# Kernel tuning notes

Hardware: AMD Instinct MI355X
Metric: run time of the kernel (lower is better)

## Reference

```python
import jax, jax.numpy as jnp
import numpy as np

B, S, E, H = 16, 1024, 320, 8
DH = E // H  # 40


def _lin(x, W, b):
    return x @ W.T + b


def setup_inputs() -> dict:
    key = jax.random.key(0)
    ks = jax.random.split(key, 16)

    def w(k, shape, fan_in):
        return jax.random.normal(k, shape, dtype=jnp.float32) / np.float32(np.sqrt(fan_in))

    z = lambda n: jnp.zeros((n,), jnp.float32)
    return {
        "sequence_features": jax.random.normal(ks[0], (B, S, E), dtype=jnp.float32),
        # feature_processor (shared, applied twice): Linear(320,320)+ReLU+Linear(320,320)
        "fpW1": w(ks[1], (E, E), E), "fpb1": z(E),
        "fpW2": w(ks[2], (E, E), E), "fpb2": z(E),
        # MultiheadAttention(320, 8) in/out projections
        "Wq": w(ks[3], (E, E), E), "bq": z(E),
        "Wk": w(ks[4], (E, E), E), "bk": z(E),
        "Wv": w(ks[5], (E, E), E), "bv": z(E),
        "Wo": w(ks[6], (E, E), E), "bo": z(E),
        # contact MLP: Linear(320,160)+ReLU+Linear(160,1)
        "mW1": w(ks[7], (160, E), E), "mb1": z(160),
        "mW2": w(ks[8], (1, 160), 160), "mb2": z(1),
        # position_predictor: Linear(640,320)+ReLU+Linear(320,160)+ReLU+Linear(160,3)
        "pW1": w(ks[9], (E, 2 * E), 2 * E), "pb1": z(E),
        "pW2": w(ks[10], (160, E), E), "pb2": z(160),
        "pW3": w(ks[11], (3, 160), 160), "pb3": z(3),
    }


def _forward(x, fpW1, fpb1, fpW2, fpb2, Wq, bq, Wk, bk, Wv, bv, Wo, bo,
             mW1, mb1, mW2, mb2, pW1, pb1, pW2, pb2, pW3, pb3):
    # feature_processor (dropout = identity in eval)
    backbone = _lin(jax.nn.relu(_lin(x, fpW1, fpb1)), fpW2, fpb2)        # [B,S,E]
    side = _lin(jax.nn.relu(_lin(backbone, fpW1, fpb1)), fpW2, fpb2)     # [B,S,E]

    # MultiheadAttention with batch_first=False semantics: input is treated as
    # [L=B, N=S, E], i.e. attention mixes over the batch axis (dim 0).
    q = _lin(x, Wq, bq).reshape(B, S, H, DH)
    k = _lin(x, Wk, bk).reshape(B, S, H, DH)
    v = _lin(x, Wv, bv).reshape(B, S, H, DH)
    scale = np.float32(1.0 / np.sqrt(DH))
    scores = jnp.einsum("lshd,mshd->shlm", q, k) * scale                 # [S,H,B,B]
    attn = jax.nn.softmax(scores, axis=-1)
    ctx = jnp.einsum("shlm,mshd->lshd", attn, v).reshape(B, S, E)
    attn_out = _lin(ctx, Wo, bo)                                         # [B,S,E]

    # per-position MLP -> scalar; torch broadcast-assigns it across the row
    prob = _lin(jax.nn.relu(_lin(attn_out, mW1, mb1)), mW2, mb2)         # [B,S,1]
    contact_map = jnp.broadcast_to(prob, (B, S, S))                      # [B,S,S]

    # refinement loop is a no-op: output == position_predictor(cat(bb, sc))
    comb = jnp.concatenate([backbone, side], axis=-1)                    # [B,S,640]
    h = jax.nn.relu(_lin(comb, pW1, pb1))
    h = jax.nn.relu(_lin(h, pW2, pb2))
    refined = _lin(h, pW3, pb3)                                          # [B,S,3]
    return backbone, side, contact_map, refined


def reference(sequence_features, fpW1, fpb1, fpW2, fpb2, Wq, bq, Wk, bk, Wv, bv,
              Wo, bo, mW1, mb1, mW2, mb2, pW1, pb1, pW2, pb2, pW3, pb3):
    return _forward(sequence_features, fpW1, fpb1, fpW2, fpb2, Wq, bq, Wk, bk,
                    Wv, bv, Wo, bo, mW1, mb1, mW2, mb2, pW1, pb1, pW2, pb2, pW3, pb3)
```

## Files before the change

### kernel.cpp

```cpp
#include <hip/hip_runtime.h>
#include <math.h>


#define M_ROWS 16384

typedef float f32x4 __attribute__((ext_vector_type(4)));
typedef __bf16 bf16x8 __attribute__((ext_vector_type(8)));
typedef unsigned short ushort_t;

typedef const __attribute__((address_space(1))) void* gas_ptr;
typedef __attribute__((address_space(3))) void* las_ptr;

__device__ __forceinline__ unsigned int f2bf(float f) {
    union { float f; unsigned int u; } v; v.f = f;
    unsigned int u = v.u + 0x7FFFu + ((v.u >> 16) & 1u);
    return u >> 16;
}
__device__ __forceinline__ float bf2f(ushort_t s) {
    union { unsigned int u; float f; } v; v.u = ((unsigned int)s) << 16;
    return v.f;
}

template<int BN>
__device__ __forceinline__ void gemm_core(
    int tx, int ty,
    const ushort_t* __restrict__ X1, const ushort_t* __restrict__ X2,
    int ksplit, int K, const ushort_t* __restrict__ W,
    char* smem, f32x4 (*acc)[2])
{
    constexpr int BM = 128, BK = 64;
    constexpr int WROWS = (BN == 64) ? 2 : 4;
    constexpr int WCOLS = 4 / WROWS;
    constexpr int WM = BM / WROWS;
    constexpr int WN = BN / WCOLS;
    constexpr int MF = WM / 16;
    constexpr int NF = WN / 16;

    ushort_t* As = (ushort_t*)smem;
    ushort_t* Bs = As + BM * BK;

    const int tid  = threadIdx.x;
    const int wave = tid >> 6;
    const int lane = tid & 63;
    const int m0 = ty * BM;
    const int n0 = tx * BN;
    const int wr = wave / WCOLS;
    const int wc = wave % WCOLS;
    const int sr = lane >> 3;
    const int su = lane & 7;

    for (int k0 = 0; k0 < K; k0 += BK) {
        #pragma unroll
        for (int i = 0; i < (BM * BK * 2) / 4096; ++i) {
            const int c = i * 4 + wave;
            const int r = c * 8 + sr;
            const int gk = k0 + (su ^ (r & 7)) * 8;
            const ushort_t* src;
            if (gk < ksplit) src = X1 + (size_t)(m0 + r) * ksplit + gk;
            else             src = X2 + (size_t)(m0 + r) * (K - ksplit) + (gk - ksplit);
            __builtin_amdgcn_global_load_lds((gas_ptr)src, (las_ptr)&As[c * 512], 16, 0, 0);
        }
        #pragma unroll
        for (int i = 0; i < (BN * BK * 2) / 4096; ++i) {
            const int c = i * 4 + wave;
            const int r = c * 8 + sr;
            const int gk = k0 + (su ^ (r & 7)) * 8;
            const ushort_t* src = W + (size_t)(n0 + r) * K + gk;
            __builtin_amdgcn_global_load_lds((gas_ptr)src, (las_ptr)&Bs[c * 512], 16, 0, 0);
        }
        __syncthreads();

        #pragma unroll
        for (int s = 0; s < 2; ++s) {
            bf16x8 a[MF], b[NF];
            #pragma unroll
            for (int mf = 0; mf < MF; ++mf) {
                const int r  = wr * WM + mf * 16 + (lane & 15);
                const int lu = (s * 4 + (lane >> 4)) ^ (r & 7);
                a[mf] = *reinterpret_cast<const bf16x8*>(&As[r * 64 + lu * 8]);
            }
            #pragma unroll
            for (int nf = 0; nf < NF; ++nf) {
                const int r  = wc * WN + nf * 16 + (lane & 15);
                const int lu = (s * 4 + (lane >> 4)) ^ (r & 7);
                b[nf] = *reinterpret_cast<const bf16x8*>(&Bs[r * 64 + lu * 8]);
            }
            #pragma unroll
            for (int mf = 0; mf < MF; ++mf)
                #pragma unroll
                for (int nf = 0; nf < NF; ++nf)
                    acc[mf][nf] = __builtin_amdgcn_mfma_f32_16x16x32_bf16(
                        a[mf], b[nf], acc[mf][nf], 0, 0, 0);
        }
        __syncthreads();
    }
}

template<int BN, bool RELU>
__device__ __forceinline__ void gemm_store(
    int tx, int ty, f32x4 (*acc)[2], const float* __restrict__ bias,
    float* __restrict__ outF, ushort_t* __restrict__ outB, int N)
{
    constexpr int WROWS = (BN == 64) ? 2 : 4;
    constexpr int WCOLS = 4 / WROWS;
    constexpr int WM = 128 / WROWS;
    constexpr int WN = BN / WCOLS;
    constexpr int MF = WM / 16;

    const int tid  = threadIdx.x;
    const int wave = tid >> 6;
    const int lane = tid & 63;
    const int wr = wave / WCOLS;
    const int wc = wave % WCOLS;

    #pragma unroll
    for (int nf = 0; nf < 2; ++nf) {
        const int gn = tx * BN + wc * WN + nf * 16 + (lane & 15);
        const float bv = bias[gn];
        #pragma unroll
        for (int mf = 0; mf < MF; ++mf) {
            #pragma unroll
            for (int i = 0; i < 4; ++i) {
                const int gm = ty * 128 + wr * WM + mf * 16 + (lane >> 4) * 4 + i;
                float v = acc[mf][nf][i] + bv;
                if (RELU) v = fmaxf(v, 0.f);
                if (outF) outF[(size_t)gm * N + gn] = v;
                if (outB) outB[(size_t)gm * N + gn] = (ushort_t)f2bf(v);
            }
        }
    }
}

template<int BN, bool RELU>
__device__ __forceinline__ void gemm_full(
    int bid, int ntx,
    const ushort_t* X1, const ushort_t* X2, int ksplit, int K,
    const ushort_t* W, const float* bias,
    float* outF, ushort_t* outB, int N, char* smem)
{
    const int tx = bid % ntx, ty = bid / ntx;
    constexpr int MF = (BN == 64) ? 4 : 2;
    f32x4 acc[MF][2];
    #pragma unroll
    for (int i = 0; i < MF; ++i) { acc[i][0] = (f32x4)0.f; acc[i][1] = (f32x4)0.f; }
    gemm_core<BN>(tx, ty, X1, X2, ksplit, K, W, smem, acc);
    gemm_store<BN, RELU>(tx, ty, acc, bias, outF, outB, N);
}

__device__ __forceinline__ void attn_dev(
    int ab, const ushort_t* __restrict__ qkv, ushort_t* __restrict__ ctx, char* smem)
{
    float* q_s = (float*)smem;
    float* k_s = q_s + 16 * 40;
    float* v_s = k_s + 16 * 40;
    float* p_s = v_s + 16 * 40;

    const int s   = ab >> 3;
    const int h   = ab & 7;
    const int tid = threadIdx.x;
    const int hb  = h * 40;

    for (int idx = tid; idx < 16 * 40; idx += 256) {
        int l = idx / 40, d = idx % 40;
        size_t row = (size_t)(l * 1024 + s) * 960;
        q_s[idx] = bf2f(qkv[row + hb + d]);
        k_s[idx] = bf2f(qkv[row + 320 + hb + d]);
        v_s[idx] = bf2f(qkv[row + 640 + hb + d]);
    }
    __syncthreads();

    {
        const int l = tid >> 4, m = tid & 15;
        float sc = 0.f;
        #pragma unroll
        for (int d = 0; d < 40; ++d) sc += q_s[l * 40 + d] * k_s[m * 40 + d];
        sc *= 0.15811388300841897f;
        float mx = sc;
        #pragma unroll
        for (int off = 1; off < 16; off <<= 1) mx = fmaxf(mx, __shfl_xor(mx, off, 16));
        float e = expf(sc - mx);
        float sum = e;
        #pragma unroll
        for (int off = 1; off < 16; off <<= 1) sum += __shfl_xor(sum, off, 16);
        p_s[l * 16 + m] = e / sum;
    }
    __syncthreads();

    for (int idx = tid; idx < 16 * 40; idx += 256) {
        int l = idx / 40, d = idx % 40;
        float acc = 0.f;
        #pragma unroll
        for (int m = 0; m < 16; ++m) acc += p_s[l * 16 + m] * v_s[m * 40 + d];
        ctx[(size_t)(l * 1024 + s) * 320 + hb + d] = (ushort_t)f2bf(acc);
    }
}


__device__ __forceinline__ void stage64(
    const ushort_t* __restrict__ src, int row0, int ldk, int k0,
    ushort_t* dst, int wave, int sr, int su)
{
    #pragma unroll
    for (int i = 0; i < 2; ++i) {
        const int c = i * 4 + wave;
        const int r = c * 8 + sr;
        const int gk = k0 + (su ^ (r & 7)) * 8;
        __builtin_amdgcn_global_load_lds(
            (gas_ptr)(src + (size_t)(row0 + r) * ldk + gk),
            (las_ptr)&dst[c * 512], 16, 0, 0);
    }
}
__device__ __forceinline__ void stage32(
    const ushort_t* __restrict__ src, int row0, int ldk, int k0,
    ushort_t* dst, int wave, int sr, int su)
{
    const int r = wave * 8 + sr;
    const int gk = k0 + (su ^ (r & 7)) * 8;
    __builtin_amdgcn_global_load_lds(
        (gas_ptr)(src + (size_t)(row0 + r) * ldk + gk),
        (las_ptr)&dst[wave * 512], 16, 0, 0);
}

__device__ void fusedB_dev(
    int panel, const ushort_t* __restrict__ bbB,
    const ushort_t* __restrict__ fpW1b, const float* __restrict__ fpb1,
    const ushort_t* __restrict__ fpW2b, const float* __restrict__ fpb2,
    float* __restrict__ out_side, ushort_t* __restrict__ sideB, char* smem)
{
    ushort_t* tpan = (ushort_t*)smem;
    ushort_t* As   = tpan + 5 * 4096;
    ushort_t* Bs   = As + 4096;

    const int tid = threadIdx.x, wave = tid >> 6, lane = tid & 63;
    const int row0 = panel * 64;
    const int wr = wave >> 1, wc = wave & 1;
    const int sr = lane >> 3, su = lane & 7;

    for (int nb = 0; nb < 5; ++nb) {
        f32x4 acc[2][2];
        acc[0][0] = acc[0][1] = acc[1][0] = acc[1][1] = (f32x4)0.f;
        for (int k0 = 0; k0 < 320; k0 += 64) {
            stage64(bbB,   row0,    320, k0, As, wave, sr, su);
            stage64(fpW1b, nb * 64, 320, k0, Bs, wave, sr, su);
            __syncthreads();
            #pragma unroll
            for (int s = 0; s < 2; ++s) {
                bf16x8 a[2], b[2];
                #pragma unroll
                for (int mf = 0; mf < 2; ++mf) {
                    const int r  = wr * 32 + mf * 16 + (lane & 15);
                    const int lu = (s * 4 + (lane >> 4)) ^ (r & 7);
                    a[mf] = *reinterpret_cast<const bf16x8*>(&As[r * 64 + lu * 8]);
                }
                #pragma unroll
                for (int nf = 0; nf < 2; ++nf) {
                    const int r  = wc * 32 + nf * 16 + (lane & 15);
                    const int lu = (s * 4 + (lane >> 4)) ^ (r & 7);
                    b[nf] = *reinterpret_cast<const bf16x8*>(&Bs[r * 64 + lu * 8]);
                }
                #pragma unroll
                for (int mf = 0; mf < 2; ++mf)
                    #pragma unroll
                    for (int nf = 0; nf < 2; ++nf)
                        acc[mf][nf] = __builtin_amdgcn_mfma_f32_16x16x32_bf16(
                            a[mf], b[nf], acc[mf][nf], 0, 0, 0);
            }
            __syncthreads();
        }
        #pragma unroll
        for (int nf = 0; nf < 2; ++nf) {
            const int col = wc * 32 + nf * 16 + (lane & 15);
            const float bv = fpb1[nb * 64 + col];
            #pragma unroll
            for (int mf = 0; mf < 2; ++mf) {
                #pragma unroll
                for (int i = 0; i < 4; ++i) {
                    const int row = wr * 32 + mf * 16 + (lane >> 4) * 4 + i;
                    float v = fmaxf(acc[mf][nf][i] + bv, 0.f);
                    const int u = col >> 3;
                    tpan[nb * 4096 + row * 64 + ((u ^ (row & 7)) * 8) + (col & 7)]
                        = (ushort_t)f2bf(v);
                }
            }
        }
        __syncthreads();
    }

    for (int nb = 0; nb < 5; ++nb) {
        f32x4 acc[2][2];
        acc[0][0] = acc[0][1] = acc[1][0] = acc[1][1] = (f32x4)0.f;
        for (int kt = 0; kt < 5; ++kt) {
            stage64(fpW2b, nb * 64, 320, kt * 64, Bs, wave, sr, su);
            __syncthreads();
            #pragma unroll
            for (int s = 0; s < 2; ++s) {
                bf16x8 a[2], b[2];
                #pragma unroll
                for (int mf = 0; mf < 2; ++mf) {
                    const int r  = wr * 32 + mf * 16 + (lane & 15);
                    const int lu = (s * 4 + (lane >> 4)) ^ (r & 7);
                    a[mf] = *reinterpret_cast<const bf16x8*>(&tpan[kt * 4096 + r * 64 + lu * 8]);
                }
                #pragma unroll
                for (int nf = 0; nf < 2; ++nf) {
                    const int r  = wc * 32 + nf * 16 + (lane & 15);
                    const int lu = (s * 4 + (lane >> 4)) ^ (r & 7);
                    b[nf] = *reinterpret_cast<const bf16x8*>(&Bs[r * 64 + lu * 8]);
                }
                #pragma unroll
                for (int mf = 0; mf < 2; ++mf)
                    #pragma unroll
                    for (int nf = 0; nf < 2; ++nf)
                        acc[mf][nf] = __builtin_amdgcn_mfma_f32_16x16x32_bf16(
                            a[mf], b[nf], acc[mf][nf], 0, 0, 0);
            }
            __syncthreads();
        }
        #pragma unroll
        for (int nf = 0; nf < 2; ++nf) {
            const int gn = nb * 64 + wc * 32 + nf * 16 + (lane & 15);
            const float bv = fpb2[gn];
            #pragma unroll
            for (int mf = 0; mf < 2; ++mf) {
                #pragma unroll
                for (int i = 0; i < 4; ++i) {
                    const int gm = row0 + wr * 32 + mf * 16 + (lane >> 4) * 4 + i;
                    float v = acc[mf][nf][i] + bv;
                    out_side[(size_t)gm * 320 + gn] = v;
                    sideB[(size_t)gm * 320 + gn] = (ushort_t)f2bf(v);
                }
            }
        }
    }
}

__device__ void fusedC_dev(
    int panel, const ushort_t* __restrict__ bbB, const ushort_t* __restrict__ sideB,
    const ushort_t* __restrict__ pW1b, const float* __restrict__ pb1,
    const ushort_t* __restrict__ pW2b, const float* __restrict__ pb2,
    const float* __restrict__ pW3, const float* __restrict__ pb3,
    float* __restrict__ out_ref, char* smem)
{
    ushort_t* tpan = (ushort_t*)smem;
    ushort_t* As   = tpan + 5 * 4096;
    ushort_t* Bs   = As + 4096;

    const int tid = threadIdx.x, wave = tid >> 6, lane = tid & 63;
    const int row0 = panel * 64;
    const int wr = wave >> 1, wc = wave & 1;
    const int sr = lane >> 3, su = lane & 7;

    for (int nb = 0; nb < 5; ++nb) {
        f32x4 acc[2][2];
        acc[0][0] = acc[0][1] = acc[1][0] = acc[1][1] = (f32x4)0.f;
        for (int k0 = 0; k0 < 640; k0 += 64) {
            #pragma unroll
            for (int i = 0; i < 2; ++i) {
                const int c = i * 4 + wave;
                const int r = c * 8 + sr;
                const int gk = k0 + (su ^ (r & 7)) * 8;
                const ushort_t* src = (gk < 320)
                    ? bbB   + (size_t)(row0 + r) * 320 + gk
                    : sideB + (size_t)(row0 + r) * 320 + (gk - 320);
                __builtin_amdgcn_global_load_lds((gas_ptr)src, (las_ptr)&As[c * 512], 16, 0, 0);
            }
            stage64(pW1b, nb * 64, 640, k0, Bs, wave, sr, su);
            __syncthreads();
            #pragma unroll
            for (int s = 0; s < 2; ++s) {
                bf16x8 a[2], b[2];
                #pragma unroll
                for (int mf = 0; mf < 2; ++mf) {
                    const int r  = wr * 32 + mf * 16 + (lane & 15);
                    const int lu = (s * 4 + (lane >> 4)) ^ (r & 7);
                    a[mf] = *reinterpret_cast<const bf16x8*>(&As[r * 64 + lu * 8]);
                }
                #pragma unroll
                for (int nf = 0; nf < 2; ++nf) {
                    const int r  = wc * 32 + nf * 16 + (lane & 15);
                    const int lu = (s * 4 + (lane >> 4)) ^ (r & 7);
                    b[nf] = *reinterpret_cast<const bf16x8*>(&Bs[r * 64 + lu * 8]);
                }
                #pragma unroll
                for (int mf = 0; mf < 2; ++mf)
                    #pragma unroll
                    for (int nf = 0; nf < 2; ++nf)
                        acc[mf][nf] = __builtin_amdgcn_mfma_f32_16x16x32_bf16(
                            a[mf], b[nf], acc[mf][nf], 0, 0, 0);
            }
            __syncthreads();
        }
        #pragma unroll
        for (int nf = 0; nf < 2; ++nf) {
            const int col = wc * 32 + nf * 16 + (lane & 15);
            const float bv = pb1[nb * 64 + col];
            #pragma unroll
            for (int mf = 0; mf < 2; ++mf) {
                #pragma unroll
                for (int i = 0; i < 4; ++i) {
                    const int row = wr * 32 + mf * 16 + (lane >> 4) * 4 + i;
                    float v = fmaxf(acc[mf][nf][i] + bv, 0.f);
                    const int u = col >> 3;
                    tpan[nb * 4096 + row * 64 + ((u ^ (row & 7)) * 8) + (col & 7)]
                        = (ushort_t)f2bf(v);
                }
            }
        }
        __syncthreads();
    }

    float part[4][3];
    #pragma unroll
    for (int i = 0; i < 4; ++i) { part[i][0] = part[i][1] = part[i][2] = 0.f; }

    for (int ct = 0; ct < 5; ++ct) {
        f32x4 acc[2];
        acc[0] = acc[1] = (f32x4)0.f;
        for (int kt = 0; kt < 5; ++kt) {
            stage32(pW2b, ct * 32, 320, kt * 64, Bs, wave, sr, su);
            __syncthreads();
            #pragma unroll
            for (int s = 0; s < 2; ++s) {
                bf16x8 a, b[2];
                {
                    const int r  = wave * 16 + (lane & 15);
                    const int lu = (s * 4 + (lane >> 4)) ^ (r & 7);
                    a = *reinterpret_cast<const bf16x8*>(&tpan[kt * 4096 + r * 64 + lu * 8]);
                }
                #pragma unroll
                for (int nf = 0; nf < 2; ++nf) {
                    const int r  = nf * 16 + (lane & 15);
                    const int lu = (s * 4 + (lane >> 4)) ^ (r & 7);
                    b[nf] = *reinterpret_cast<const bf16x8*>(&Bs[r * 64 + lu * 8]);
                }
                #pragma unroll
                for (int nf = 0; nf < 2; ++nf)
                    acc[nf] = __builtin_amdgcn_mfma_f32_16x16x32_bf16(a, b[nf], acc[nf], 0, 0, 0);
            }
            __syncthreads();
        }
        #pragma unroll
        for (int nf = 0; nf < 2; ++nf) {
            const int col = ct * 32 + nf * 16 + (lane & 15);
            const float bv = pb2[col];
            #pragma unroll
            for (int i = 0; i < 4; ++i) {
                float v = fmaxf(acc[nf][i] + bv, 0.f);
                #pragma unroll
                for (int n = 0; n < 3; ++n)
                    part[i][n] += v * pW3[n * 160 + col];
            }
        }
    }
    #pragma unroll
    for (int off = 8; off; off >>= 1)
        #pragma unroll
        for (int i = 0; i < 4; ++i)
            #pragma unroll
            for (int n = 0; n < 3; ++n)
                part[i][n] += __shfl_xor(part[i][n], off, 16);
    if ((lane & 15) == 0) {
        #pragma unroll
        for (int i = 0; i < 4; ++i) {
            const int row = row0 + wave * 16 + (lane >> 4) * 4 + i;
            #pragma unroll
            for (int n = 0; n < 3; ++n)
                out_ref[(size_t)row * 3 + n] = part[i][n] + pb3[n];
        }
    }
}

__device__ void fusedD_dev(
    int panel, const ushort_t* __restrict__ aoB,
    const ushort_t* __restrict__ mW1b, const float* __restrict__ mb1,
    const float* __restrict__ mW2, const float* __restrict__ mb2,
    float* __restrict__ out_cm, char* smem)
{
    ushort_t* As = (ushort_t*)smem;
    ushort_t* Bs = As + 4096;
    float* probs = (float*)(Bs + 2048);

    const int tid = threadIdx.x, wave = tid >> 6, lane = tid & 63;
    const int row0 = panel * 64;
    const int sr = lane >> 3, su = lane & 7;

    float part[4] = {0.f, 0.f, 0.f, 0.f};

    for (int ct = 0; ct < 5; ++ct) {
        f32x4 acc[2];
        acc[0] = acc[1] = (f32x4)0.f;
        for (int k0 = 0; k0 < 320; k0 += 64) {
            stage64(aoB,  row0,    320, k0, As, wave, sr, su);
            stage32(mW1b, ct * 32, 320, k0, Bs, wave, sr, su);
            __syncthreads();
            #pragma unroll
            for (int s = 0; s < 2; ++s) {
                bf16x8 a, b[2];
                {
                    const int r  = wave * 16 + (lane & 15);
                    const int lu = (s * 4 + (lane >> 4)) ^ (r & 7);
                    a = *reinterpret_cast<const bf16x8*>(&As[r * 64 + lu * 8]);
                }
                #pragma unroll
                for (int nf = 0; nf < 2; ++nf) {
                    const int r  = nf * 16 + (lane & 15);
                    const int lu = (s * 4 + (lane >> 4)) ^ (r & 7);
                    b[nf] = *reinterpret_cast<const bf16x8*>(&Bs[r * 64 + lu * 8]);
                }
                #pragma unroll
                for (int nf = 0; nf < 2; ++nf)
                    acc[nf] = __builtin_amdgcn_mfma_f32_16x16x32_bf16(a, b[nf], acc[nf], 0, 0, 0);
            }
            __syncthreads();
        }
        #pragma unroll
        for (int nf = 0; nf < 2; ++nf) {
            const int col = ct * 32 + nf * 16 + (lane & 15);
            const float bv = mb1[col];
            const float w  = mW2[col];
            #pragma unroll
            for (int i = 0; i < 4; ++i)
                part[i] += fmaxf(acc[nf][i] + bv, 0.f) * w;
        }
    }
    #pragma unroll
    for (int off = 8; off; off >>= 1)
        #pragma unroll
        for (int i = 0; i < 4; ++i)
            part[i] += __shfl_xor(part[i], off, 16);
    if ((lane & 15) == 0) {
        #pragma unroll
        for (int i = 0; i < 4; ++i)
            probs[wave * 16 + (lane >> 4) * 4 + i] = part[i] + mb2[0];
    }
    __syncthreads();

    for (int r = 0; r < 64; ++r) {
        const float p = probs[r];
        reinterpret_cast<float4*>(out_cm + (size_t)(row0 + r) * 1024)[tid] =
            make_float4(p, p, p, p);
    }
}


struct ConvDesc { const float* src; ushort_t* dst; };
struct ConvPack { ConvDesc d[10]; int start[11]; };

__global__ __launch_bounds__(256) void conv_all(ConvPack p)
{
    const int bid = blockIdx.x;
    int i = 0;
    #pragma unroll
    for (int t = 0; t < 10; ++t) if (bid >= p.start[t + 1]) i = t + 1;
    const int local = bid - p.start[i];
    const int idx = (local * 256 + (int)threadIdx.x) * 4;
    float4 v = *reinterpret_cast<const float4*>(&p.d[i].src[idx]);
    unsigned int lo = f2bf(v.x) | (f2bf(v.y) << 16);
    unsigned int hi = f2bf(v.z) | (f2bf(v.w) << 16);
    *reinterpret_cast<uint2*>(&p.d[i].dst[idx]) = make_uint2(lo, hi);
}

__global__ __launch_bounds__(256) void k_g1(
    const ushort_t* __restrict__ xb, const ushort_t* __restrict__ Wcat,
    const float* __restrict__ fpb1, const float* __restrict__ bq,
    const float* __restrict__ bk, const float* __restrict__ bvv,
    ushort_t* __restrict__ t1b, ushort_t* __restrict__ qkvb)
{
    __shared__ __align__(16) char smem[24 * 1024];
    const int bid = blockIdx.x;
    const int tx = bid % 20, ty = bid / 20;
    f32x4 acc[4][2];
    #pragma unroll
    for (int i = 0; i < 4; ++i) { acc[i][0] = (f32x4)0.f; acc[i][1] = (f32x4)0.f; }
    gemm_core<64>(tx, ty, xb, xb, 320, 320, Wcat, smem, acc);

    const int tid = threadIdx.x, wave = tid >> 6, lane = tid & 63;
    const int wr = wave >> 1, wc = wave & 1;
    #pragma unroll
    for (int nf = 0; nf < 2; ++nf) {
        const int gn = tx * 64 + wc * 32 + nf * 16 + (lane & 15);
        float bv;
        if      (gn < 320) bv = fpb1[gn];
        else if (gn < 640) bv = bq[gn - 320];
        else if (gn < 960) bv = bk[gn - 640];
        else               bv = bvv[gn - 960];
        #pragma unroll
        for (int mf = 0; mf < 4; ++mf) {
            #pragma unroll
            for (int i = 0; i < 4; ++i) {
                const int gm = ty * 128 + wr * 64 + mf * 16 + (lane >> 4) * 4 + i;
                float v = acc[mf][nf][i] + bv;
                if (gn < 320) t1b [(size_t)gm * 320 + gn] = (ushort_t)f2bf(fmaxf(v, 0.f));
                else          qkvb[(size_t)gm * 960 + gn - 320] = (ushort_t)f2bf(v);
            }
        }
    }
}

__global__ __launch_bounds__(256) void k_g2_attn(
    const ushort_t* __restrict__ t1b, const ushort_t* __restrict__ fpW2b,
    const float* __restrict__ fpb2, float* __restrict__ out_bb,
    ushort_t* __restrict__ bbB,
    const ushort_t* __restrict__ qkvb, ushort_t* __restrict__ ctxb)
{
    __shared__ __align__(16) char smem[24 * 1024];
    const int bid = blockIdx.x;
    if (bid < 640) gemm_full<64, false>(bid, 5, t1b, t1b, 320, 320, fpW2b, fpb2, out_bb, bbB, 320, smem);
    else           attn_dev(bid - 640, qkvb, ctxb, smem);
}

__global__ __launch_bounds__(256) void k_l3(
    const ushort_t* __restrict__ bbB,
    const ushort_t* __restrict__ fpW1b, const float* __restrict__ fpb1,
    const ushort_t* __restrict__ fpW2b, const float* __restrict__ fpb2,
    float* __restrict__ out_side, ushort_t* __restrict__ sideB,
    const ushort_t* __restrict__ ctxb, const ushort_t* __restrict__ Wob,
    const float* __restrict__ bo, ushort_t* __restrict__ aoB)
{
    __shared__ __align__(16) char smem[56 * 1024];
    const int bid = blockIdx.x;
    if (bid < 256) fusedB_dev(bid, bbB, fpW1b, fpb1, fpW2b, fpb2, out_side, sideB, smem);
    else           gemm_full<64, false>(bid - 256, 5, ctxb, ctxb, 320, 320, Wob, bo, nullptr, aoB, 320, smem);
}

__global__ __launch_bounds__(256) void k_l4(
    const ushort_t* __restrict__ bbB, const ushort_t* __restrict__ sideB,
    const ushort_t* __restrict__ pW1b, const float* __restrict__ pb1,
    const ushort_t* __restrict__ pW2b, const float* __restrict__ pb2,
    const float* __restrict__ pW3, const float* __restrict__ pb3,
    float* __restrict__ out_ref,
    const ushort_t* __restrict__ aoB,
    const ushort_t* __restrict__ mW1b, const float* __restrict__ mb1,
    const float* __restrict__ mW2, const float* __restrict__ mb2,
    float* __restrict__ out_cm)
{
    __shared__ __align__(16) char smem[56 * 1024];
    const int bid = blockIdx.x;
    if (bid < 256) fusedC_dev(bid, bbB, sideB, pW1b, pb1, pW2b, pb2, pW3, pb3, out_ref, smem);
    else           fusedD_dev(bid - 256, aoB, mW1b, mb1, mW2, mb2, out_cm, smem);
}

extern "C" void kernel_launch(void* const* d_in, const int* in_sizes, int n_in,
                              void* d_out, int out_size, void* d_ws, size_t ws_size,
                              hipStream_t stream)
{
    const float* x    = (const float*)d_in[0];
    const float* fpW1 = (const float*)d_in[1];
    const float* fpb1 = (const float*)d_in[2];
    const float* fpW2 = (const float*)d_in[3];
    const float* fpb2 = (const float*)d_in[4];
    const float* Wq   = (const float*)d_in[5];
    const float* bq   = (const float*)d_in[6];
    const float* Wk   = (const float*)d_in[7];
    const float* bk   = (const float*)d_in[8];
    const float* Wv   = (const float*)d_in[9];
    const float* bv   = (const float*)d_in[10];
    const float* Wo   = (const float*)d_in[11];
    const float* bo   = (const float*)d_in[12];
    const float* mW1  = (const float*)d_in[13];
    const float* mb1  = (const float*)d_in[14];
    const float* mW2  = (const float*)d_in[15];
    const float* mb2  = (const float*)d_in[16];
    const float* pW1  = (const float*)d_in[17];
    const float* pb1  = (const float*)d_in[18];
    const float* pW2  = (const float*)d_in[19];
    const float* pb2  = (const float*)d_in[20];
    const float* pW3  = (const float*)d_in[21];
    const float* pb3  = (const float*)d_in[22];

    float* out      = (float*)d_out;
    float* out_bb   = out;
    float* out_side = out + 5242880;
    float* out_cm   = out + 2 * 5242880;
    float* out_ref  = out + 2 * 5242880 + 16777216;

    ushort_t* ws = (ushort_t*)d_ws;
    const size_t BUF = 5242880;
    ushort_t* xb    = ws;
    ushort_t* t1b   = ws + 1 * BUF;
    ushort_t* bbB   = ws + 2 * BUF;
    ushort_t* sideB = ws + 3 * BUF;
    ushort_t* qkvb  = ws + 4 * BUF;
    ushort_t* wb    = ws + 7 * BUF;
    ushort_t* fpW1b = wb;
    ushort_t* Wqb   = wb + 102400;
    ushort_t* Wkb   = wb + 204800;
    ushort_t* Wvb   = wb + 307200;
    ushort_t* fpW2b = wb + 409600;
    ushort_t* Wob   = wb + 512000;
    ushort_t* mW1b  = wb + 614400;
    ushort_t* pW1b  = wb + 665600;
    ushort_t* pW2b  = wb + 870400;

    ushort_t* ctxb = xb;
    ushort_t* aoB  = qkvb;

    dim3 blk(256);

    ConvPack cp;
    const float* srcs[10] = {x, fpW1, Wq, Wk, Wv, fpW2, Wo, mW1, pW1, pW2};
    ushort_t*    dsts[10] = {xb, fpW1b, Wqb, Wkb, Wvb, fpW2b, Wob, mW1b, pW1b, pW2b};
    const int    nblk[10] = {5120, 100, 100, 100, 100, 100, 100, 50, 200, 50};
    int acc_blk = 0;
    for (int i = 0; i < 10; ++i) {
        cp.d[i].src = srcs[i]; cp.d[i].dst = dsts[i];
        cp.start[i] = acc_blk; acc_blk += nblk[i];
    }
    cp.start[10] = acc_blk;
    conv_all<<<dim3(acc_blk), blk, 0, stream>>>(cp);

    k_g1<<<dim3(2560), blk, 0, stream>>>(xb, wb, fpb1, bq, bk, bv, t1b, qkvb);
    k_g2_attn<<<dim3(8832), blk, 0, stream>>>(t1b, fpW2b, fpb2, out_bb, bbB, qkvb, ctxb);
    k_l3<<<dim3(896), blk, 0, stream>>>(bbB, fpW1b, fpb1, fpW2b, fpb2,
                                        out_side, sideB, ctxb, Wob, bo, aoB);
    k_l4<<<dim3(512), blk, 0, stream>>>(bbB, sideB, pW1b, pb1, pW2b, pb2, pW3, pb3,
                                        out_ref, aoB, mW1b, mb1, mW2, mb2, out_cm);
}
```

Baseline: 162.5 us.

## Split fused position-predictor kernel into a parallel GEMM stage and a tail kernel

The first position-predictor layer (640->320 with ReLU) is moved out of the per-panel fused kernel and run as a generic tiled GEMM over 640 blocks that writes a bf16 intermediate to workspace. The remaining layers run in a new small kernel that loads that intermediate into shared memory. The aim is more parallelism than 256 panel blocks each serially computing five column tiles, at the cost of an extra launch and a global round trip for the intermediate. Shared memory for k_l4 also drops to 24 KB, which may raise occupancy.

```diff
diff --git a/kernel.cpp b/kernel.cpp
--- a/kernel.cpp
+++ b/kernel.cpp
@@ -334,80 +334,23 @@
     }
 }
 
-__device__ void fusedC_dev(
-    int panel, const ushort_t* __restrict__ bbB, const ushort_t* __restrict__ sideB,
-    const ushort_t* __restrict__ pW1b, const float* __restrict__ pb1,
+__device__ void fusedC2_dev(
+    int panel, const ushort_t* __restrict__ t3,
     const ushort_t* __restrict__ pW2b, const float* __restrict__ pb2,
     const float* __restrict__ pW3, const float* __restrict__ pb3,
     float* __restrict__ out_ref, char* smem)
 {
     ushort_t* tpan = (ushort_t*)smem;
-    ushort_t* As   = tpan + 5 * 4096;
-    ushort_t* Bs   = As + 4096;
+    ushort_t* Bs   = tpan + 5 * 4096;
 
     const int tid = threadIdx.x, wave = tid >> 6, lane = tid & 63;
     const int row0 = panel * 64;
-    const int wr = wave >> 1, wc = wave & 1;
     const int sr = lane >> 3, su = lane & 7;
 
-    for (int nb = 0; nb < 5; ++nb) {
-        f32x4 acc[2][2];
-        acc[0][0] = acc[0][1] = acc[1][0] = acc[1][1] = (f32x4)0.f;
-        for (int k0 = 0; k0 < 640; k0 += 64) {
-            #pragma unroll
-            for (int i = 0; i < 2; ++i) {
-                const int c = i * 4 + wave;
-                const int r = c * 8 + sr;
-                const int gk = k0 + (su ^ (r & 7)) * 8;
-                const ushort_t* src = (gk < 320)
-                    ? bbB   + (size_t)(row0 + r) * 320 + gk
-                    : sideB + (size_t)(row0 + r) * 320 + (gk - 320);
-                __builtin_amdgcn_global_load_lds((gas_ptr)src, (las_ptr)&As[c * 512], 16, 0, 0);
-            }
-            stage64(pW1b, nb * 64, 640, k0, Bs, wave, sr, su);
-            __syncthreads();
-            #pragma unroll
-            for (int s = 0; s < 2; ++s) {
-                bf16x8 a[2], b[2];
-                #pragma unroll
-                for (int mf = 0; mf < 2; ++mf) {
-                    const int r  = wr * 32 + mf * 16 + (lane & 15);
-                    const int lu = (s * 4 + (lane >> 4)) ^ (r & 7);
-                    a[mf] = *reinterpret_cast<const bf16x8*>(&As[r * 64 + lu * 8]);
-                }
-                #pragma unroll
-                for (int nf = 0; nf < 2; ++nf) {
-                    const int r  = wc * 32 + nf * 16 + (lane & 15);
-                    const int lu = (s * 4 + (lane >> 4)) ^ (r & 7);
-                    b[nf] = *reinterpret_cast<const bf16x8*>(&Bs[r * 64 + lu * 8]);
-                }
-                #pragma unroll
-                for (int mf = 0; mf < 2; ++mf)
-                    #pragma unroll
-                    for (int nf = 0; nf < 2; ++nf)
-                        acc[mf][nf] = __builtin_amdgcn_mfma_f32_16x16x32_bf16(
-                            a[mf], b[nf], acc[mf][nf], 0, 0, 0);
-            }
-            __syncthreads();
-        }
-        #pragma unroll
-        for (int nf = 0; nf < 2; ++nf) {
-            const int col = wc * 32 + nf * 16 + (lane & 15);
-            const float bv = pb1[nb * 64 + col];
-            #pragma unroll
-            for (int mf = 0; mf < 2; ++mf) {
-                #pragma unroll
-                for (int i = 0; i < 4; ++i) {
-                    const int row = wr * 32 + mf * 16 + (lane >> 4) * 4 + i;
-                    float v = fmaxf(acc[mf][nf][i] + bv, 0.f);
-                    const int u = col >> 3;
-                    tpan[nb * 4096 + row * 64 + ((u ^ (row & 7)) * 8) + (col & 7)]
-                        = (ushort_t)f2bf(v);
-                }
-            }
-        }
-        __syncthreads();
-    }
+    #pragma unroll
+    for (int kt = 0; kt < 5; ++kt)
+        stage64(t3, row0, 320, kt * 64, tpan + kt * 4096, wave, sr, su);
+    __syncthreads();
 
     float part[4][3];
     #pragma unroll
@@ -626,18 +569,26 @@
 __global__ __launch_bounds__(256) void k_l4(
     const ushort_t* __restrict__ bbB, const ushort_t* __restrict__ sideB,
     const ushort_t* __restrict__ pW1b, const float* __restrict__ pb1,
-    const ushort_t* __restrict__ pW2b, const float* __restrict__ pb2,
-    const float* __restrict__ pW3, const float* __restrict__ pb3,
-    float* __restrict__ out_ref,
+    ushort_t* __restrict__ t3,
     const ushort_t* __restrict__ aoB,
     const ushort_t* __restrict__ mW1b, const float* __restrict__ mb1,
     const float* __restrict__ mW2, const float* __restrict__ mb2,
     float* __restrict__ out_cm)
 {
-    __shared__ __align__(16) char smem[56 * 1024];
+    __shared__ __align__(16) char smem[24 * 1024];
     const int bid = blockIdx.x;
-    if (bid < 256) fusedC_dev(bid, bbB, sideB, pW1b, pb1, pW2b, pb2, pW3, pb3, out_ref, smem);
-    else           fusedD_dev(bid - 256, aoB, mW1b, mb1, mW2, mb2, out_cm, smem);
+    if (bid < 640) gemm_full<64, true>(bid, 5, bbB, sideB, 320, 640, pW1b, pb1, nullptr, t3, 320, smem);
+    else           fusedD_dev(bid - 640, aoB, mW1b, mb1, mW2, mb2, out_cm, smem);
+}
+
+__global__ __launch_bounds__(256) void k_l5(
+    const ushort_t* __restrict__ t3,
+    const ushort_t* __restrict__ pW2b, const float* __restrict__ pb2,
+    const float* __restrict__ pW3, const float* __restrict__ pb3,
+    float* __restrict__ out_ref)
+{
+    __shared__ __align__(16) char smem[48 * 1024];
+    fusedC2_dev(blockIdx.x, t3, pW2b, pb2, pW3, pb3, out_ref, smem);
 }
 
 extern "C" void kernel_launch(void* const* d_in, const int* in_sizes, int n_in,
@@ -694,6 +645,7 @@
 
     ushort_t* ctxb = xb;
     ushort_t* aoB  = qkvb;
+    ushort_t* t3   = t1b;
 
     dim3 blk(256);
 
@@ -713,6 +665,7 @@
     k_g2_attn<<<dim3(8832), blk, 0, stream>>>(t1b, fpW2b, fpb2, out_bb, bbB, qkvb, ctxb);
     k_l3<<<dim3(896), blk, 0, stream>>>(bbB, fpW1b, fpb1, fpW2b, fpb2,
                                         out_side, sideB, ctxb, Wob, bo, aoB);
-    k_l4<<<dim3(512), blk, 0, stream>>>(bbB, sideB, pW1b, pb1, pW2b, pb2, pW3, pb3,
-                                        out_ref, aoB, mW1b, mb1, mW2, mb2, out_cm);
-}
+    k_l4<<<dim3(896), blk, 0, stream>>>(bbB, sideB, pW1b, pb1, t3,
+                                        aoB, mW1b, mb1, mW2, mb2, out_cm);
+    k_l5<<<dim3(256), blk, 0, stream>>>(t3, pW2b, pb2, pW3, pb3, out_ref);
+}
```

Result: slower. 168.2 us (+3.5%).

## Halve fused-MLP row panels to 32 and overlap late weight conversion with first GEMM

Applied to the files above, without the earlier changes.

The fused side-feature and position-predictor kernels now process 32-row panels instead of 64, doubling block count (512 vs 256) and cutting shared memory from 56KB to 32/34KB so more blocks fit per CU. The position predictor's final 3-wide projection is now reduced across wave columns through a small shared buffer. Weight conversions not needed by the first GEMM are moved out of the standalone conversion kernel and appended as extra blocks of k_g1, running alongside it. In exchange, each weight tile is re-staged for twice as many panels, so weight traffic per output row goes up.

```diff
diff --git a/kernel.cpp b/kernel.cpp
--- a/kernel.cpp
+++ b/kernel.cpp
@@ -221,36 +221,34 @@
         (las_ptr)&dst[wave * 512], 16, 0, 0);
 }
 
-__device__ void fusedB_dev(
+__device__ void fusedB32_dev(
     int panel, const ushort_t* __restrict__ bbB,
     const ushort_t* __restrict__ fpW1b, const float* __restrict__ fpb1,
     const ushort_t* __restrict__ fpW2b, const float* __restrict__ fpb2,
     float* __restrict__ out_side, ushort_t* __restrict__ sideB, char* smem)
 {
     ushort_t* tpan = (ushort_t*)smem;
-    ushort_t* As   = tpan + 5 * 4096;
-    ushort_t* Bs   = As + 4096;
+    ushort_t* As   = tpan + 5 * 2048;
+    ushort_t* Bs   = As + 2048;
 
     const int tid = threadIdx.x, wave = tid >> 6, lane = tid & 63;
-    const int row0 = panel * 64;
+    const int row0 = panel * 32;
     const int wr = wave >> 1, wc = wave & 1;
     const int sr = lane >> 3, su = lane & 7;
 
     for (int nb = 0; nb < 5; ++nb) {
-        f32x4 acc[2][2];
-        acc[0][0] = acc[0][1] = acc[1][0] = acc[1][1] = (f32x4)0.f;
+        f32x4 acc[2]; acc[0] = (f32x4)0.f; acc[1] = (f32x4)0.f;
         for (int k0 = 0; k0 < 320; k0 += 64) {
-            stage64(bbB,   row0,    320, k0, As, wave, sr, su);
+            stage32(bbB,   row0,    320, k0, As, wave, sr, su);
             stage64(fpW1b, nb * 64, 320, k0, Bs, wave, sr, su);
             __syncthreads();
             #pragma unroll
             for (int s = 0; s < 2; ++s) {
-                bf16x8 a[2], b[2];
-                #pragma unroll
-                for (int mf = 0; mf < 2; ++mf) {
-                    const int r  = wr * 32 + mf * 16 + (lane & 15);
-                    const int lu = (s * 4 + (lane >> 4)) ^ (r & 7);
-                    a[mf] = *reinterpret_cast<const bf16x8*>(&As[r * 64 + lu * 8]);
+                bf16x8 a, b[2];
+                {
+                    const int r  = wr * 16 + (lane & 15);
+                    const int lu = (s * 4 + (lane >> 4)) ^ (r & 7);
+                    a = *reinterpret_cast<const bf16x8*>(&As[r * 64 + lu * 8]);
                 }
                 #pragma unroll
                 for (int nf = 0; nf < 2; ++nf) {
@@ -259,11 +257,8 @@
                     b[nf] = *reinterpret_cast<const bf16x8*>(&Bs[r * 64 + lu * 8]);
                 }
                 #pragma unroll
-                for (int mf = 0; mf < 2; ++mf)
-                    #pragma unroll
-                    for (int nf = 0; nf < 2; ++nf)
-                        acc[mf][nf] = __builtin_amdgcn_mfma_f32_16x16x32_bf16(
-                            a[mf], b[nf], acc[mf][nf], 0, 0, 0);
+                for (int nf = 0; nf < 2; ++nf)
+                    acc[nf] = __builtin_amdgcn_mfma_f32_16x16x32_bf16(a, b[nf], acc[nf], 0, 0, 0);
             }
             __syncthreads();
         }
@@ -272,34 +267,29 @@
             const int col = wc * 32 + nf * 16 + (lane & 15);
             const float bv = fpb1[nb * 64 + col];
             #pragma unroll
-            for (int mf = 0; mf < 2; ++mf) {
-                #pragma unroll
-                for (int i = 0; i < 4; ++i) {
-                    const int row = wr * 32 + mf * 16 + (lane >> 4) * 4 + i;
-                    float v = fmaxf(acc[mf][nf][i] + bv, 0.f);
-                    const int u = col >> 3;
-                    tpan[nb * 4096 + row * 64 + ((u ^ (row & 7)) * 8) + (col & 7)]
-                        = (ushort_t)f2bf(v);
-                }
+            for (int i = 0; i < 4; ++i) {
+                const int row = wr * 16 + (lane >> 4) * 4 + i;
+                float v = fmaxf(acc[nf][i] + bv, 0.f);
+                const int u = col >> 3;
+                tpan[nb * 2048 + row * 64 + ((u ^ (row & 7)) * 8) + (col & 7)]
+                    = (ushort_t)f2bf(v);
             }
         }
         __syncthreads();
     }
 
     for (int nb = 0; nb < 5; ++nb) {
-        f32x4 acc[2][2];
-        acc[0][0] = acc[0][1] = acc[1][0] = acc[1][1] = (f32x4)0.f;
+        f32x4 acc[2]; acc[0] = (f32x4)0.f; acc[1] = (f32x4)0.f;
         for (int kt = 0; kt < 5; ++kt) {
             stage64(fpW2b, nb * 64, 320, kt * 64, Bs, wave, sr, su);
             __syncthreads();
             #pragma unroll
             for (int s = 0; s < 2; ++s) {
-                bf16x8 a[2], b[2];
-                #pragma unroll
-                for (int mf = 0; mf < 2; ++mf) {
-                    const int r  = wr * 32 + mf * 16 + (lane & 15);
-                    const int lu = (s * 4 + (lane >> 4)) ^ (r & 7);
-                    a[mf] = *reinterpret_cast<const bf16x8*>(&tpan[kt * 4096 + r * 64 + lu * 8]);
+                bf16x8 a, b[2];
+                {
+                    const int r  = wr * 16 + (lane & 15);
+                    const int lu = (s * 4 + (lane >> 4)) ^ (r & 7);
+                    a = *reinterpret_cast<const bf16x8*>(&tpan[kt * 2048 + r * 64 + lu * 8]);
                 }
                 #pragma unroll
                 for (int nf = 0; nf < 2; ++nf) {
@@ -308,11 +298,8 @@
                     b[nf] = *reinterpret_cast<const bf16x8*>(&Bs[r * 64 + lu * 8]);
                 }
                 #pragma unroll
-                for (int mf = 0; mf < 2; ++mf)
-                    #pragma unroll
-                    for (int nf = 0; nf < 2; ++nf)
-                        acc[mf][nf] = __builtin_amdgcn_mfma_f32_16x16x32_bf16(
-                            a[mf], b[nf], acc[mf][nf], 0, 0, 0);
+                for (int nf = 0; nf < 2; ++nf)
+                    acc[nf] = __builtin_amdgcn_mfma_f32_16x16x32_bf16(a, b[nf], acc[nf], 0, 0, 0);
             }
             __syncthreads();
         }
@@ -321,20 +308,17 @@
             const int gn = nb * 64 + wc * 32 + nf * 16 + (lane & 15);
             const float bv = fpb2[gn];
             #pragma unroll
-            for (int mf = 0; mf < 2; ++mf) {
-                #pragma unroll
-                for (int i = 0; i < 4; ++i) {
-                    const int gm = row0 + wr * 32 + mf * 16 + (lane >> 4) * 4 + i;
-                    float v = acc[mf][nf][i] + bv;
-                    out_side[(size_t)gm * 320 + gn] = v;
-                    sideB[(size_t)gm * 320 + gn] = (ushort_t)f2bf(v);
-                }
-            }
-        }
-    }
-}
-
-__device__ void fusedC_dev(
+            for (int i = 0; i < 4; ++i) {
+                const int gm = row0 + wr * 16 + (lane >> 4) * 4 + i;
+                float v = acc[nf][i] + bv;
+                out_side[(size_t)gm * 320 + gn] = v;
+                sideB[(size_t)gm * 320 + gn] = (ushort_t)f2bf(v);
+            }
+        }
+    }
+}
+
+__device__ void fusedC32_dev(
     int panel, const ushort_t* __restrict__ bbB, const ushort_t* __restrict__ sideB,
     const ushort_t* __restrict__ pW1b, const float* __restrict__ pb1,
     const ushort_t* __restrict__ pW2b, const float* __restrict__ pb2,
@@ -342,38 +326,35 @@
     float* __restrict__ out_ref, char* smem)
 {
     ushort_t* tpan = (ushort_t*)smem;
-    ushort_t* As   = tpan + 5 * 4096;
-    ushort_t* Bs   = As + 4096;
+    ushort_t* As   = tpan + 5 * 2048;
+    ushort_t* Bs   = As + 2048;
+    float*    pSum = (float*)(Bs + 4096);
 
     const int tid = threadIdx.x, wave = tid >> 6, lane = tid & 63;
-    const int row0 = panel * 64;
+    const int row0 = panel * 32;
     const int wr = wave >> 1, wc = wave & 1;
     const int sr = lane >> 3, su = lane & 7;
 
     for (int nb = 0; nb < 5; ++nb) {
-        f32x4 acc[2][2];
-        acc[0][0] = acc[0][1] = acc[1][0] = acc[1][1] = (f32x4)0.f;
+        f32x4 acc[2]; acc[0] = (f32x4)0.f; acc[1] = (f32x4)0.f;
         for (int k0 = 0; k0 < 640; k0 += 64) {
-            #pragma unroll
-            for (int i = 0; i < 2; ++i) {
-                const int c = i * 4 + wave;
-                const int r = c * 8 + sr;
+            {
+                const int r = wave * 8 + sr;
                 const int gk = k0 + (su ^ (r & 7)) * 8;
                 const ushort_t* src = (gk < 320)
                     ? bbB   + (size_t)(row0 + r) * 320 + gk
                     : sideB + (size_t)(row0 + r) * 320 + (gk - 320);
-                __builtin_amdgcn_global_load_lds((gas_ptr)src, (las_ptr)&As[c * 512], 16, 0, 0);
+                __builtin_amdgcn_global_load_lds((gas_ptr)src, (las_ptr)&As[wave * 512], 16, 0, 0);
             }
             stage64(pW1b, nb * 64, 640, k0, Bs, wave, sr, su);
             __syncthreads();
             #pragma unroll
             for (int s = 0; s < 2; ++s) {
-                bf16x8 a[2], b[2];
-                #pragma unroll
-                for (int mf = 0; mf < 2; ++mf) {
-                    const int r  = wr * 32 + mf * 16 + (lane & 15);
-                    const int lu = (s * 4 + (lane >> 4)) ^ (r & 7);
-                    a[mf] = *reinterpret_cast<const bf16x8*>(&As[r * 64 + lu * 8]);
+                bf16x8 a, b[2];
+                {
+                    const int r  = wr * 16 + (lane & 15);
+                    const int lu = (s * 4 + (lane >> 4)) ^ (r & 7);
+                    a = *reinterpret_cast<const bf16x8*>(&As[r * 64 + lu * 8]);
                 }
                 #pragma unroll
                 for (int nf = 0; nf < 2; ++nf) {
@@ -382,11 +363,8 @@
                     b[nf] = *reinterpret_cast<const bf16x8*>(&Bs[r * 64 + lu * 8]);
                 }
                 #pragma unroll
-                for (int mf = 0; mf < 2; ++mf)
-                    #pragma unroll
-                    for (int nf = 0; nf < 2; ++nf)
-                        acc[mf][nf] = __builtin_amdgcn_mfma_f32_16x16x32_bf16(
-                            a[mf], b[nf], acc[mf][nf], 0, 0, 0);
+                for (int nf = 0; nf < 2; ++nf)
+                    acc[nf] = __builtin_amdgcn_mfma_f32_16x16x32_bf16(a, b[nf], acc[nf], 0, 0, 0);
             }
             __syncthreads();
         }
@@ -395,15 +373,12 @@
             const int col = wc * 32 + nf * 16 + (lane & 15);
             const float bv = pb1[nb * 64 + col];
             #pragma unroll
-            for (int mf = 0; mf < 2; ++mf) {
-                #pragma unroll
-                for (int i = 0; i < 4; ++i) {
-                    const int row = wr * 32 + mf * 16 + (lane >> 4) * 4 + i;
-                    float v = fmaxf(acc[mf][nf][i] + bv, 0.f);
-                    const int u = col >> 3;
-                    tpan[nb * 4096 + row * 64 + ((u ^ (row & 7)) * 8) + (col & 7)]
-                        = (ushort_t)f2bf(v);
-                }
+            for (int i = 0; i < 4; ++i) {
+                const int row = wr * 16 + (lane >> 4) * 4 + i;
+                float v = fmaxf(acc[nf][i] + bv, 0.f);
+                const int u = col >> 3;
+                tpan[nb * 2048 + row * 64 + ((u ^ (row & 7)) * 8) + (col & 7)]
+                    = (ushort_t)f2bf(v);
             }
         }
         __syncthreads();
@@ -414,42 +389,35 @@
     for (int i = 0; i < 4; ++i) { part[i][0] = part[i][1] = part[i][2] = 0.f; }
 
     for (int ct = 0; ct < 5; ++ct) {
-        f32x4 acc[2];
-        acc[0] = acc[1] = (f32x4)0.f;
+        f32x4 acc = (f32x4)0.f;
         for (int kt = 0; kt < 5; ++kt) {
             stage32(pW2b, ct * 32, 320, kt * 64, Bs, wave, sr, su);
             __syncthreads();
             #pragma unroll
             for (int s = 0; s < 2; ++s) {
-                bf16x8 a, b[2];
+                bf16x8 a, b;
                 {
-                    const int r  = wave * 16 + (lane & 15);
-                    const int lu = (s * 4 + (lane >> 4)) ^ (r & 7);
-                    a = *reinterpret_cast<const bf16x8*>(&tpan[kt * 4096 + r * 64 + lu * 8]);
-                }
-                #pragma unroll
-                for (int nf = 0; nf < 2; ++nf) {
-                    const int r  = nf * 16 + (lane & 15);
-                    const int lu = (s * 4 + (lane >> 4)) ^ (r & 7);
-                    b[nf] = *reinterpret_cast<const bf16x8*>(&Bs[r * 64 + lu * 8]);
-                }
-                #pragma unroll
-                for (int nf = 0; nf < 2; ++nf)
-                    acc[nf] = __builtin_amdgcn_mfma_f32_16x16x32_bf16(a, b[nf], acc[nf], 0, 0, 0);
-            }
-            __syncthreads();
-        }
-        #pragma unroll
-        for (int nf = 0; nf < 2; ++nf) {
-            const int col = ct * 32 + nf * 16 + (lane & 15);
-            const float bv = pb2[col];
-            #pragma unroll
-            for (int i = 0; i < 4; ++i) {
-                float v = fmaxf(acc[nf][i] + bv, 0.f);
-                #pragma unroll
-                for (int n = 0; n < 3; ++n)
-                    part[i][n] += v * pW3[n * 160 + col];
-            }
+                    const int r  = wr * 16 + (lane & 15);
+                    const int lu = (s * 4 + (lane >> 4)) ^ (r & 7);
+                    a = *reinterpret_cast<const bf16x8*>(&tpan[kt * 2048 + r * 64 + lu * 8]);
+                }
+                {
+                    const int r  = wc * 16 + (lane & 15);
+                    const int lu = (s * 4 + (lane >> 4)) ^ (r & 7);
+                    b = *reinterpret_cast<const bf16x8*>(&Bs[r * 64 + lu * 8]);
+                }
+                acc = __builtin_amdgcn_mfma_f32_16x16x32_bf16(a, b, acc, 0, 0, 0);
+            }
+            __syncthreads();
+        }
+        const int col = ct * 32 + wc * 16 + (lane & 15);
+        const float bv = pb2[col];
+        #pragma unroll
+        for (int i = 0; i < 4; ++i) {
+            float v = fmaxf(acc[i] + bv, 0.f);
+            #pragma unroll
+            for (int n = 0; n < 3; ++n)
+                part[i][n] += v * pW3[n * 160 + col];
         }
     }
     #pragma unroll
@@ -462,11 +430,17 @@
     if ((lane & 15) == 0) {
         #pragma unroll
         for (int i = 0; i < 4; ++i) {
-            const int row = row0 + wave * 16 + (lane >> 4) * 4 + i;
+            const int row = wr * 16 + (lane >> 4) * 4 + i;
             #pragma unroll
             for (int n = 0; n < 3; ++n)
-                out_ref[(size_t)row * 3 + n] = part[i][n] + pb3[n];
-        }
+                pSum[(wc * 32 + row) * 3 + n] = part[i][n];
+        }
+    }
+    __syncthreads();
+    if (tid < 96) {
+        const int row = tid / 3, n = tid % 3;
+        out_ref[(size_t)(row0 + row) * 3 + n] =
+            pSum[row * 3 + n] + pSum[(32 + row) * 3 + n] + pb3[n];
     }
 }
 
@@ -544,30 +518,35 @@
 
 
 struct ConvDesc { const float* src; ushort_t* dst; };
-struct ConvPack { ConvDesc d[10]; int start[11]; };
-
-__global__ __launch_bounds__(256) void conv_all(ConvPack p)
-{
-    const int bid = blockIdx.x;
+struct ConvPack { ConvDesc d[5]; int start[6]; };
+
+__device__ __forceinline__ void conv_unit(const ConvPack& p, int u, int tid)
+{
     int i = 0;
     #pragma unroll
-    for (int t = 0; t < 10; ++t) if (bid >= p.start[t + 1]) i = t + 1;
-    const int local = bid - p.start[i];
-    const int idx = (local * 256 + (int)threadIdx.x) * 4;
+    for (int t = 0; t < 5; ++t) if (u >= p.start[t + 1]) i = t + 1;
+    const int idx = ((u - p.start[i]) * 256 + tid) * 4;
     float4 v = *reinterpret_cast<const float4*>(&p.d[i].src[idx]);
     unsigned int lo = f2bf(v.x) | (f2bf(v.y) << 16);
     unsigned int hi = f2bf(v.z) | (f2bf(v.w) << 16);
     *reinterpret_cast<uint2*>(&p.d[i].dst[idx]) = make_uint2(lo, hi);
 }
 
+__global__ __launch_bounds__(256) void conv_k(ConvPack p)
+{
+    conv_unit(p, blockIdx.x, threadIdx.x);
+}
+
 __global__ __launch_bounds__(256) void k_g1(
     const ushort_t* __restrict__ xb, const ushort_t* __restrict__ Wcat,
     const float* __restrict__ fpb1, const float* __restrict__ bq,
     const float* __restrict__ bk, const float* __restrict__ bvv,
-    ushort_t* __restrict__ t1b, ushort_t* __restrict__ qkvb)
+    ushort_t* __restrict__ t1b, ushort_t* __restrict__ qkvb, ConvPack cp)
 {
     __shared__ __align__(16) char smem[24 * 1024];
     const int bid = blockIdx.x;
+    if (bid >= 2560) { conv_unit(cp, bid - 2560, threadIdx.x); return; }
+
     const int tx = bid % 20, ty = bid / 20;
     f32x4 acc[4][2];
     #pragma unroll
@@ -617,10 +596,10 @@
     const ushort_t* __restrict__ ctxb, const ushort_t* __restrict__ Wob,
     const float* __restrict__ bo, ushort_t* __restrict__ aoB)
 {
-    __shared__ __align__(16) char smem[56 * 1024];
+    __shared__ __align__(16) char smem[32 * 1024];
     const int bid = blockIdx.x;
-    if (bid < 256) fusedB_dev(bid, bbB, fpW1b, fpb1, fpW2b, fpb2, out_side, sideB, smem);
-    else           gemm_full<64, false>(bid - 256, 5, ctxb, ctxb, 320, 320, Wob, bo, nullptr, aoB, 320, smem);
+    if (bid < 512) fusedB32_dev(bid, bbB, fpW1b, fpb1, fpW2b, fpb2, out_side, sideB, smem);
+    else           gemm_full<64, false>(bid - 512, 5, ctxb, ctxb, 320, 320, Wob, bo, nullptr, aoB, 320, smem);
 }
 
 __global__ __launch_bounds__(256) void k_l4(
@@ -634,10 +613,10 @@
     const float* __restrict__ mW2, const float* __restrict__ mb2,
     float* __restrict__ out_cm)
 {
-    __shared__ __align__(16) char smem[56 * 1024];
+    __shared__ __align__(16) char smem[34 * 1024];
     const int bid = blockIdx.x;
-    if (bid < 256) fusedC_dev(bid, bbB, sideB, pW1b, pb1, pW2b, pb2, pW3, pb3, out_ref, smem);
-    else           fusedD_dev(bid - 256, aoB, mW1b, mb1, mW2, mb2, out_cm, smem);
+    if (bid < 512) fusedC32_dev(bid, bbB, sideB, pW1b, pb1, pW2b, pb2, pW3, pb3, out_ref, smem);
+    else           fusedD_dev(bid - 512, aoB, mW1b, mb1, mW2, mb2, out_cm, smem);
 }
 
 extern "C" void kernel_launch(void* const* d_in, const int* in_sizes, int n_in,
@@ -697,22 +676,31 @@
 
     dim3 blk(256);
 
-    ConvPack cp;
-    const float* srcs[10] = {x, fpW1, Wq, Wk, Wv, fpW2, Wo, mW1, pW1, pW2};
-    ushort_t*    dsts[10] = {xb, fpW1b, Wqb, Wkb, Wvb, fpW2b, Wob, mW1b, pW1b, pW2b};
-    const int    nblk[10] = {5120, 100, 100, 100, 100, 100, 100, 50, 200, 50};
-    int acc_blk = 0;
-    for (int i = 0; i < 10; ++i) {
-        cp.d[i].src = srcs[i]; cp.d[i].dst = dsts[i];
-        cp.start[i] = acc_blk; acc_blk += nblk[i];
-    }
-    cp.start[10] = acc_blk;
-    conv_all<<<dim3(acc_blk), blk, 0, stream>>>(cp);
-
-    k_g1<<<dim3(2560), blk, 0, stream>>>(xb, wb, fpb1, bq, bk, bv, t1b, qkvb);
+    ConvPack cp0;
+    {
+        const float* s[5] = {x, fpW1, Wq, Wk, Wv};
+        ushort_t*    d[5] = {xb, fpW1b, Wqb, Wkb, Wvb};
+        const int    n[5] = {5120, 100, 100, 100, 100};
+        int a = 0;
+        for (int i = 0; i < 5; ++i) { cp0.d[i] = {s[i], d[i]}; cp0.start[i] = a; a += n[i]; }
+        cp0.start[5] = a;
+    }
+    conv_k<<<dim3(5520), blk, 0, stream>>>(cp0);
+
+    ConvPack cp1;
+    {
+        const float* s[5] = {fpW2, Wo, mW1, pW1, pW2};
+        ushort_t*    d[5] = {fpW2b, Wob, mW1b, pW1b, pW2b};
+        const int    n[5] = {100, 100, 50, 200, 50};
+        int a = 0;
+        for (int i = 0; i < 5; ++i) { cp1.d[i] = {s[i], d[i]}; cp1.start[i] = a; a += n[i]; }
+        cp1.start[5] = a;
+    }
+    k_g1<<<dim3(2560 + 500), blk, 0, stream>>>(xb, wb, fpb1, bq, bk, bv, t1b, qkvb, cp1);
+
     k_g2_attn<<<dim3(8832), blk, 0, stream>>>(t1b, fpW2b, fpb2, out_bb, bbB, qkvb, ctxb);
-    k_l3<<<dim3(896), blk, 0, stream>>>(bbB, fpW1b, fpb1, fpW2b, fpb2,
-                                        out_side, sideB, ctxb, Wob, bo, aoB);
-    k_l4<<<dim3(512), blk, 0, stream>>>(bbB, sideB, pW1b, pb1, pW2b, pb2, pW3, pb3,
+    k_l3<<<dim3(1152), blk, 0, stream>>>(bbB, fpW1b, fpb1, fpW2b, fpb2,
+                                         out_side, sideB, ctxb, Wob, bo, aoB);
+    k_l4<<<dim3(768), blk, 0, stream>>>(bbB, sideB, pW1b, pb1, pW2b, pb2, pW3, pb3,
                                         out_ref, aoB, mW1b, mb1, mW2, mb2, out_cm);
 }
```

New measurement: 157.9 us. 2.8% less time.
